# Kernel tuning notes

Hardware: AMD Instinct MI355X
Metric: run time of the kernel (lower is better)

The kernel has to match this reference:

```python
import jax, jax.numpy as jnp
import numpy as np

B, C, H, W = 2, 16, 160, 192
S, D = 3, 48
MIN_DEPTH, MAX_DEPTH = 0.5, 10.0
EPS = 1e-6


def setup_inputs() -> dict:
    key = jax.random.key(0)
    k1, k2 = jax.random.split(key)
    ref_feats = jax.random.normal(k1, (B, C, H, W), jnp.float32)
    src_feats = jax.random.normal(k2, (S, B, C, H, W), jnp.float32)
    K = np.array([[200.0, 0.0, W / 2.0], [0.0, 200.0, H / 2.0], [0.0, 0.0, 1.0]], np.float32)
    ref_intrinsics = jnp.broadcast_to(jnp.asarray(K), (B, 3, 3))
    src_intrinsics = jnp.broadcast_to(jnp.asarray(K), (S, B, 3, 3))
    T = np.tile(np.eye(4, dtype=np.float32), (S, B, 1, 1))
    T[:, :, 0, 3] = np.array([0.15, -0.15, 0.05], np.float32)[:, None]  # x baselines
    T[:, :, 1, 3] = 0.05  # small y offset
    ref_to_src = jnp.asarray(T)
    depth_hypotheses = jnp.linspace(MIN_DEPTH, MAX_DEPTH, D, dtype=jnp.float32)
    return {"ref_feats": ref_feats, "src_feats": src_feats,
            "ref_intrinsics": ref_intrinsics, "src_intrinsics": src_intrinsics,
            "ref_to_src": ref_to_src, "depth_hypotheses": depth_hypotheses}


def _bilinear(img, x, y, valid):
    """img: [B,C,Hs,Ws]; x,y,valid: [B,D,N]. Zero padding outside. -> [B,C,D,N]"""
    Hs, Ws = img.shape[2], img.shape[3]
    x0 = jnp.floor(x); y0 = jnp.floor(y)
    fx = x - x0; fy = y - y0
    x0i = x0.astype(jnp.int32); y0i = y0.astype(jnp.int32)
    gather = jax.vmap(lambda im, yy, xx: im[:, yy, xx])  # per-batch [C,D,N]
    out = jnp.zeros(img.shape[:2] + x.shape[1:], img.dtype)
    for dy in (0, 1):
        for dx in (0, 1):
            xi = x0i + dx; yi = y0i + dy
            w = (fx if dx else 1.0 - fx) * (fy if dy else 1.0 - fy)
            ok = valid & (xi >= 0) & (xi < Ws) & (yi >= 0) & (yi < Hs)
            vals = gather(img, jnp.clip(yi, 0, Hs - 1), jnp.clip(xi, 0, Ws - 1))
            out = out + vals * jnp.where(ok, w, 0.0)[:, None]
    return out


def _ncc(f1, f2, eps=EPS):
    """NCC over channel axis 1. f1: [B,C,1,H,W], f2: [B,C,D,H,W] -> [B,D,H,W]"""
    f1 = f1 - f1.mean(axis=1, keepdims=True)
    f2 = f2 - f2.mean(axis=1, keepdims=True)
    num = (f1 * f2).sum(axis=1)
    den = jnp.sqrt((f1 * f1).sum(axis=1)) * jnp.sqrt((f2 * f2).sum(axis=1)) + eps
    return num / den


def reference(ref_feats, src_feats, ref_intrinsics, src_intrinsics, ref_to_src, depth_hypotheses):
    b, c, h, w = ref_feats.shape
    s = src_feats.shape[0]
    us, vs = jnp.meshgrid(jnp.arange(w, dtype=jnp.float32), jnp.arange(h, dtype=jnp.float32))  # [h,w]
    pix = jnp.stack([us.ravel(), vs.ravel(), jnp.ones(h * w, jnp.float32)], axis=0)  # [3,HW]
    rays = jnp.einsum('bij,jn->bin', jnp.linalg.inv(ref_intrinsics), pix)  # [B,3,HW]
    X = depth_hypotheses[None, :, None, None] * rays[:, None]  # [B,D,3,HW]
    cost = jnp.zeros((b, depth_hypotheses.shape[0], h, w), ref_feats.dtype)
    for si in range(s):
        R = ref_to_src[si, :, :3, :3]; t = ref_to_src[si, :, :3, 3]
        Xs = jnp.einsum('bij,bdjn->bdin', R, X) + t[:, None, :, None]  # [B,D,3,HW]
        p = jnp.einsum('bij,bdjn->bdin', src_intrinsics[si], Xs)
        z = p[:, :, 2]
        valid = z > 1e-3
        zs = jnp.maximum(z, 1e-3)
        x = p[:, :, 0] / zs; y = p[:, :, 1] / zs  # [B,D,HW]
        warped = _bilinear(src_feats[si], x, y, valid).reshape(b, c, -1, h, w)  # [B,C,D,H,W]
        cost = cost + _ncc(ref_feats[:, :, None], warped)
    return cost / s
```

## Files before the change

kernel.cpp:

```cpp
#include <hip/hip_runtime.h>
#include <math.h>

constexpr int B = 2, C = 16, H = 160, W = 192, S = 3, D = 48;
constexpr int HW = H * W;

__global__ __launch_bounds__(256) void plane_sweep_kernel(
    const float* __restrict__ ref_feats,
    const float* __restrict__ src_feats,
    const float* __restrict__ ref_intr,
    const float* __restrict__ src_intr,
    const float* __restrict__ ref_to_src,
    const float* __restrict__ depths,
    float* __restrict__ out)
{
    const int idx = blockIdx.x * blockDim.x + threadIdx.x;
    const int total = B * D * HW;
    if (idx >= total) return;

    const int w = idx % W;
    const int h = (idx / W) % H;
    const int d = (idx / HW) % D;
    const int b = idx / (HW * D);

    const float* Kp = ref_intr + b * 9;
    const double a00 = Kp[0], a01 = Kp[1], a02 = Kp[2];
    const double a10 = Kp[3], a11 = Kp[4], a12 = Kp[5];
    const double a20 = Kp[6], a21 = Kp[7], a22 = Kp[8];
    const double cof00 =  (a11 * a22 - a12 * a21);
    const double cof01 = -(a10 * a22 - a12 * a20);
    const double cof02 =  (a10 * a21 - a11 * a20);
    const double cof10 = -(a01 * a22 - a02 * a21);
    const double cof11 =  (a00 * a22 - a02 * a20);
    const double cof12 = -(a00 * a21 - a01 * a20);
    const double cof20 =  (a01 * a12 - a02 * a11);
    const double cof21 = -(a00 * a12 - a02 * a10);
    const double cof22 =  (a00 * a11 - a01 * a10);
    const double det = a00 * cof00 + a01 * cof01 + a02 * cof02;
    const double invdet = 1.0 / det;
    const double i00 = cof00 * invdet, i01 = cof10 * invdet, i02 = cof20 * invdet;
    const double i10 = cof01 * invdet, i11 = cof11 * invdet, i12 = cof21 * invdet;
    const double i20 = cof02 * invdet, i21 = cof12 * invdet, i22 = cof22 * invdet;

    const double u = (double)w;
    const double v = (double)h;
    const double rayx = i00 * u + i01 * v + i02;
    const double rayy = i10 * u + i11 * v + i12;
    const double rayz = i20 * u + i21 * v + i22;

    const double depth = (double)depths[d];
    const double X0 = depth * rayx;
    const double X1 = depth * rayy;
    const double X2 = depth * rayz;

    float f1[C];
    const float* rp = ref_feats + (b * C) * HW + h * W + w;
    float sum1 = 0.0f;
    #pragma unroll
    for (int c = 0; c < C; ++c) {
        f1[c] = rp[c * HW];
        sum1 += f1[c];
    }
    const float m1 = sum1 * (1.0f / C);
    float sq1 = 0.0f;
    #pragma unroll
    for (int c = 0; c < C; ++c) {
        f1[c] -= m1;
        sq1 += f1[c] * f1[c];
    }
    const float n1 = sqrtf(sq1);

    float cost = 0.0f;

    for (int s = 0; s < S; ++s) {
        const float* Tp  = ref_to_src + (s * B + b) * 16;
        const float* Ksp = src_intr   + (s * B + b) * 9;

        const double Xsx = (double)Tp[0] * X0 + (double)Tp[1] * X1 + (double)Tp[2]  * X2 + (double)Tp[3];
        const double Xsy = (double)Tp[4] * X0 + (double)Tp[5] * X1 + (double)Tp[6]  * X2 + (double)Tp[7];
        const double Xsz = (double)Tp[8] * X0 + (double)Tp[9] * X1 + (double)Tp[10] * X2 + (double)Tp[11];

        const double p0 = (double)Ksp[0] * Xsx + (double)Ksp[1] * Xsy + (double)Ksp[2] * Xsz;
        const double p1 = (double)Ksp[3] * Xsx + (double)Ksp[4] * Xsy + (double)Ksp[5] * Xsz;
        const double p2 = (double)Ksp[6] * Xsx + (double)Ksp[7] * Xsy + (double)Ksp[8] * Xsz;

        const bool valid = p2 > 0.001;
        const double zs = fmax(p2, 0.001);
        const double invz = 1.0 / zs;
        const double x = p0 * invz;
        const double y = p1 * invz;

        const double x0f = floor(x);
        const double y0f = floor(y);
        const double fx = x - x0f;
        const double fy = y - y0f;
        const int x0 = (int)x0f;
        const int y0 = (int)y0f;
        const int x1 = x0 + 1;
        const int y1 = y0 + 1;

        double dw00 = (1.0 - fx) * (1.0 - fy);
        double dw01 = fx * (1.0 - fy);
        double dw10 = (1.0 - fx) * fy;
        double dw11 = fx * fy;
        const bool okx0 = (x0 >= 0) && (x0 < W);
        const bool okx1 = (x1 >= 0) && (x1 < W);
        const bool oky0 = (y0 >= 0) && (y0 < H);
        const bool oky1 = (y1 >= 0) && (y1 < H);
        const float w00 = (float)((valid && okx0 && oky0) ? dw00 : 0.0);
        const float w01 = (float)((valid && okx1 && oky0) ? dw01 : 0.0);
        const float w10 = (float)((valid && okx0 && oky1) ? dw10 : 0.0);
        const float w11 = (float)((valid && okx1 && oky1) ? dw11 : 0.0);

        const int x0c = min(max(x0, 0), W - 1);
        const int x1c = min(max(x1, 0), W - 1);
        const int y0c = min(max(y0, 0), H - 1);
        const int y1c = min(max(y1, 0), H - 1);

        const int off00 = y0c * W + x0c;
        const int off01 = y0c * W + x1c;
        const int off10 = y1c * W + x0c;
        const int off11 = y1c * W + x1c;

        const float* base = src_feats + ((size_t)(s * B + b) * C) * HW;

        float f2[C];
        float sum2 = 0.0f;
        #pragma unroll
        for (int c = 0; c < C; ++c) {
            const float* p = base + c * HW;
            const float v00 = p[off00];
            const float v01 = p[off01];
            const float v10 = p[off10];
            const float v11 = p[off11];
            const float val = w00 * v00 + w01 * v01 + w10 * v10 + w11 * v11;
            f2[c] = val;
            sum2 += val;
        }
        const float m2 = sum2 * (1.0f / C);
        float sq2 = 0.0f;
        float dot = 0.0f;
        #pragma unroll
        for (int c = 0; c < C; ++c) {
            const float f2c = f2[c] - m2;
            sq2 = fmaf(f2c, f2c, sq2);
            dot = fmaf(f1[c], f2c, dot);
        }
        const float den = n1 * sqrtf(sq2) + 1e-6f;
        cost += dot / den;
    }

    out[idx] = cost * (1.0f / S);
}

extern "C" void kernel_launch(void* const* d_in, const int* in_sizes, int n_in,
                              void* d_out, int out_size, void* d_ws, size_t ws_size,
                              hipStream_t stream) {
    const float* ref_feats  = (const float*)d_in[0];
    const float* src_feats  = (const float*)d_in[1];
    const float* ref_intr   = (const float*)d_in[2];
    const float* src_intr   = (const float*)d_in[3];
    const float* ref_to_src = (const float*)d_in[4];
    const float* depths     = (const float*)d_in[5];
    float* out = (float*)d_out;

    const int total = B * D * H * W;
    const int block = 256;
    const int grid = (total + block - 1) / block;
    plane_sweep_kernel<<<grid, block, 0, stream>>>(
        ref_feats, src_feats, ref_intr, src_intr, ref_to_src, depths, out);
}
```

Before: 185.4 us.

## Precompute combined projection matrices and process four depths per thread

Adds a tiny kernel that folds K_src·R·K_ref^-1 and K_src·t into per-(source,batch) 3x4 double matrices, so each pixel computes its projection as depth*ray + offset. Each thread now handles four depth hypotheses, reusing the reference-feature load, the normalization and the per-source ray setup across them. The double division is replaced by a hardware reciprocal with two Newton refinements. In exchange it cuts thread count fourfold, which may reduce memory-latency hiding for the gathers, and adds an extra kernel launch. Regrouping the arithmetic may also round slightly differently from the reference.

```diff
diff --git a/kernel.cpp b/kernel.cpp
--- a/kernel.cpp
+++ b/kernel.cpp
@@ -3,153 +3,183 @@
 
 constexpr int B = 2, C = 16, H = 160, W = 192, S = 3, D = 48;
 constexpr int HW = H * W;
-
-__global__ __launch_bounds__(256) void plane_sweep_kernel(
-    const float* __restrict__ ref_feats,
-    const float* __restrict__ src_feats,
-    const float* __restrict__ ref_intr,
-    const float* __restrict__ src_intr,
-    const float* __restrict__ ref_to_src,
-    const float* __restrict__ depths,
-    float* __restrict__ out)
+constexpr int ND = 4;
+constexpr int G = D / ND;
+
+__global__ void precompute_mats(const float* __restrict__ ref_intr,
+                                const float* __restrict__ src_intr,
+                                const float* __restrict__ ref_to_src,
+                                double* __restrict__ ws)
 {
-    const int idx = blockIdx.x * blockDim.x + threadIdx.x;
-    const int total = B * D * HW;
-    if (idx >= total) return;
-
-    const int w = idx % W;
-    const int h = (idx / W) % H;
-    const int d = (idx / HW) % D;
-    const int b = idx / (HW * D);
+    const int i = threadIdx.x;
+    if (i >= S * B) return;
+    const int b = i % B;
 
     const float* Kp = ref_intr + b * 9;
     const double a00 = Kp[0], a01 = Kp[1], a02 = Kp[2];
     const double a10 = Kp[3], a11 = Kp[4], a12 = Kp[5];
     const double a20 = Kp[6], a21 = Kp[7], a22 = Kp[8];
-    const double cof00 =  (a11 * a22 - a12 * a21);
-    const double cof01 = -(a10 * a22 - a12 * a20);
-    const double cof02 =  (a10 * a21 - a11 * a20);
-    const double cof10 = -(a01 * a22 - a02 * a21);
-    const double cof11 =  (a00 * a22 - a02 * a20);
-    const double cof12 = -(a00 * a21 - a01 * a20);
-    const double cof20 =  (a01 * a12 - a02 * a11);
-    const double cof21 = -(a00 * a12 - a02 * a10);
-    const double cof22 =  (a00 * a11 - a01 * a10);
-    const double det = a00 * cof00 + a01 * cof01 + a02 * cof02;
-    const double invdet = 1.0 / det;
-    const double i00 = cof00 * invdet, i01 = cof10 * invdet, i02 = cof20 * invdet;
-    const double i10 = cof01 * invdet, i11 = cof11 * invdet, i12 = cof21 * invdet;
-    const double i20 = cof02 * invdet, i21 = cof12 * invdet, i22 = cof22 * invdet;
-
-    const double u = (double)w;
-    const double v = (double)h;
-    const double rayx = i00 * u + i01 * v + i02;
-    const double rayy = i10 * u + i11 * v + i12;
-    const double rayz = i20 * u + i21 * v + i22;
-
-    const double depth = (double)depths[d];
-    const double X0 = depth * rayx;
-    const double X1 = depth * rayy;
-    const double X2 = depth * rayz;
+    const double c00 =  (a11 * a22 - a12 * a21);
+    const double c01 = -(a10 * a22 - a12 * a20);
+    const double c02 =  (a10 * a21 - a11 * a20);
+    const double c10 = -(a01 * a22 - a02 * a21);
+    const double c11 =  (a00 * a22 - a02 * a20);
+    const double c12 = -(a00 * a21 - a01 * a20);
+    const double c20 =  (a01 * a12 - a02 * a11);
+    const double c21 = -(a00 * a12 - a02 * a10);
+    const double c22 =  (a00 * a11 - a01 * a10);
+    const double invdet = 1.0 / (a00 * c00 + a01 * c01 + a02 * c02);
+    const double iK[9] = { c00 * invdet, c10 * invdet, c20 * invdet,
+                           c01 * invdet, c11 * invdet, c21 * invdet,
+                           c02 * invdet, c12 * invdet, c22 * invdet };
+
+    const float* Tp = ref_to_src + i * 16;
+    const float* Ks = src_intr + i * 9;
+
+    double M[9];
+    #pragma unroll
+    for (int r = 0; r < 3; ++r)
+        #pragma unroll
+        for (int c = 0; c < 3; ++c)
+            M[r * 3 + c] = (double)Tp[r * 4 + 0] * iK[0 + c]
+                         + (double)Tp[r * 4 + 1] * iK[3 + c]
+                         + (double)Tp[r * 4 + 2] * iK[6 + c];
+
+    double* o = ws + i * 12;
+    #pragma unroll
+    for (int r = 0; r < 3; ++r) {
+        #pragma unroll
+        for (int c = 0; c < 3; ++c)
+            o[r * 3 + c] = (double)Ks[r * 3 + 0] * M[0 + c]
+                         + (double)Ks[r * 3 + 1] * M[3 + c]
+                         + (double)Ks[r * 3 + 2] * M[6 + c];
+        o[9 + r] = (double)Ks[r * 3 + 0] * (double)Tp[3]
+                 + (double)Ks[r * 3 + 1] * (double)Tp[7]
+                 + (double)Ks[r * 3 + 2] * (double)Tp[11];
+    }
+}
+
+__global__ __launch_bounds__(256) void plane_sweep_kernel(
+    const float* __restrict__ ref_feats,
+    const float* __restrict__ src_feats,
+    const float* __restrict__ depths,
+    const double* __restrict__ ws,
+    float* __restrict__ out)
+{
+    const int idx = blockIdx.x * blockDim.x + threadIdx.x;
+    const int total = B * G * HW;
+    if (idx >= total) return;
+
+    const int w  = idx % W;
+    const int h  = (idx / W) % H;
+    const int dg = (idx / HW) % G;
+    const int b  = idx / (HW * G);
 
     float f1[C];
     const float* rp = ref_feats + (b * C) * HW + h * W + w;
     float sum1 = 0.0f;
     #pragma unroll
-    for (int c = 0; c < C; ++c) {
-        f1[c] = rp[c * HW];
-        sum1 += f1[c];
-    }
+    for (int c = 0; c < C; ++c) { f1[c] = rp[c * HW]; sum1 += f1[c]; }
     const float m1 = sum1 * (1.0f / C);
     float sq1 = 0.0f;
     #pragma unroll
-    for (int c = 0; c < C; ++c) {
-        f1[c] -= m1;
-        sq1 += f1[c] * f1[c];
+    for (int c = 0; c < C; ++c) { f1[c] -= m1; sq1 = fmaf(f1[c], f1[c], sq1); }
+    const float n1 = sqrtf(sq1);
+
+    const double u = (double)w, v = (double)h;
+    double rx[S], ry[S], rz[S], q0[S], q1[S], q2[S];
+    #pragma unroll
+    for (int s = 0; s < S; ++s) {
+        const double* Aq = ws + (s * B + b) * 12;
+        rx[s] = Aq[0] * u + Aq[1] * v + Aq[2];
+        ry[s] = Aq[3] * u + Aq[4] * v + Aq[5];
+        rz[s] = Aq[6] * u + Aq[7] * v + Aq[8];
+        q0[s] = Aq[9]; q1[s] = Aq[10]; q2[s] = Aq[11];
     }
-    const float n1 = sqrtf(sq1);
-
-    float cost = 0.0f;
-
-    for (int s = 0; s < S; ++s) {
-        const float* Tp  = ref_to_src + (s * B + b) * 16;
-        const float* Ksp = src_intr   + (s * B + b) * 9;
-
-        const double Xsx = (double)Tp[0] * X0 + (double)Tp[1] * X1 + (double)Tp[2]  * X2 + (double)Tp[3];
-        const double Xsy = (double)Tp[4] * X0 + (double)Tp[5] * X1 + (double)Tp[6]  * X2 + (double)Tp[7];
-        const double Xsz = (double)Tp[8] * X0 + (double)Tp[9] * X1 + (double)Tp[10] * X2 + (double)Tp[11];
-
-        const double p0 = (double)Ksp[0] * Xsx + (double)Ksp[1] * Xsy + (double)Ksp[2] * Xsz;
-        const double p1 = (double)Ksp[3] * Xsx + (double)Ksp[4] * Xsy + (double)Ksp[5] * Xsz;
-        const double p2 = (double)Ksp[6] * Xsx + (double)Ksp[7] * Xsy + (double)Ksp[8] * Xsz;
-
-        const bool valid = p2 > 0.001;
-        const double zs = fmax(p2, 0.001);
-        const double invz = 1.0 / zs;
-        const double x = p0 * invz;
-        const double y = p1 * invz;
-
-        const double x0f = floor(x);
-        const double y0f = floor(y);
-        const double fx = x - x0f;
-        const double fy = y - y0f;
-        const int x0 = (int)x0f;
-        const int y0 = (int)y0f;
-        const int x1 = x0 + 1;
-        const int y1 = y0 + 1;
-
-        double dw00 = (1.0 - fx) * (1.0 - fy);
-        double dw01 = fx * (1.0 - fy);
-        double dw10 = (1.0 - fx) * fy;
-        double dw11 = fx * fy;
-        const bool okx0 = (x0 >= 0) && (x0 < W);
-        const bool okx1 = (x1 >= 0) && (x1 < W);
-        const bool oky0 = (y0 >= 0) && (y0 < H);
-        const bool oky1 = (y1 >= 0) && (y1 < H);
-        const float w00 = (float)((valid && okx0 && oky0) ? dw00 : 0.0);
-        const float w01 = (float)((valid && okx1 && oky0) ? dw01 : 0.0);
-        const float w10 = (float)((valid && okx0 && oky1) ? dw10 : 0.0);
-        const float w11 = (float)((valid && okx1 && oky1) ? dw11 : 0.0);
-
-        const int x0c = min(max(x0, 0), W - 1);
-        const int x1c = min(max(x1, 0), W - 1);
-        const int y0c = min(max(y0, 0), H - 1);
-        const int y1c = min(max(y1, 0), H - 1);
-
-        const int off00 = y0c * W + x0c;
-        const int off01 = y0c * W + x1c;
-        const int off10 = y1c * W + x0c;
-        const int off11 = y1c * W + x1c;
-
-        const float* base = src_feats + ((size_t)(s * B + b) * C) * HW;
-
-        float f2[C];
-        float sum2 = 0.0f;
+
+    float* op = out + (size_t)((b * D + dg * ND) * HW + h * W + w);
+
+    #pragma unroll 1
+    for (int j = 0; j < ND; ++j) {
+        const double depth = (double)depths[dg * ND + j];
+        float cost = 0.0f;
+
         #pragma unroll
-        for (int c = 0; c < C; ++c) {
-            const float* p = base + c * HW;
-            const float v00 = p[off00];
-            const float v01 = p[off01];
-            const float v10 = p[off10];
-            const float v11 = p[off11];
-            const float val = w00 * v00 + w01 * v01 + w10 * v10 + w11 * v11;
-            f2[c] = val;
-            sum2 += val;
+        for (int s = 0; s < S; ++s) {
+            const double p0 = fma(depth, rx[s], q0[s]);
+            const double p1 = fma(depth, ry[s], q1[s]);
+            const double p2 = fma(depth, rz[s], q2[s]);
+
+            const bool valid = p2 > 0.001;
+            const double zs = fmax(p2, 0.001);
+#if __has_builtin(__builtin_amdgcn_rcp)
+            double r = __builtin_amdgcn_rcp(zs);
+#else
+            double r = (double)__builtin_amdgcn_rcpf((float)zs);
+#endif
+            r = r * fma(-zs, r, 2.0);
+            r = r * fma(-zs, r, 2.0);
+            const double x = p0 * r;
+            const double y = p1 * r;
+
+            const double x0f = floor(x);
+            const double y0f = floor(y);
+            const double fx = x - x0f;
+            const double fy = y - y0f;
+            const int x0 = (int)x0f;
+            const int y0 = (int)y0f;
+            const int x1 = x0 + 1;
+            const int y1 = y0 + 1;
+
+            const double gx = 1.0 - fx, gy = 1.0 - fy;
+            const bool okx0 = (x0 >= 0) & (x0 < W);
+            const bool okx1 = (x1 >= 0) & (x1 < W);
+            const bool oky0 = (y0 >= 0) & (y0 < H);
+            const bool oky1 = (y1 >= 0) & (y1 < H);
+            const float w00 = (float)((valid & okx0 & oky0) ? gx * gy : 0.0);
+            const float w01 = (float)((valid & okx1 & oky0) ? fx * gy : 0.0);
+            const float w10 = (float)((valid & okx0 & oky1) ? gx * fy : 0.0);
+            const float w11 = (float)((valid & okx1 & oky1) ? fx * fy : 0.0);
+
+            const int x0c = min(max(x0, 0), W - 1);
+            const int x1c = min(max(x1, 0), W - 1);
+            const int y0c = min(max(y0, 0), H - 1);
+            const int y1c = min(max(y1, 0), H - 1);
+            const int off00 = y0c * W + x0c;
+            const int off01 = y0c * W + x1c;
+            const int off10 = y1c * W + x0c;
+            const int off11 = y1c * W + x1c;
+
+            const float* base = src_feats + ((size_t)(s * B + b) * C) * HW;
+
+            float f2[C];
+            float sum2 = 0.0f;
+            #pragma unroll
+            for (int c = 0; c < C; ++c) {
+                const float* p = base + c * HW;
+                const float v00 = p[off00];
+                const float v01 = p[off01];
+                const float v10 = p[off10];
+                const float v11 = p[off11];
+                const float val = w00 * v00 + w01 * v01 + w10 * v10 + w11 * v11;
+                f2[c] = val;
+                sum2 += val;
+            }
+            const float m2 = sum2 * (1.0f / C);
+            float sq2 = 0.0f;
+            float dot = 0.0f;
+            #pragma unroll
+            for (int c = 0; c < C; ++c) {
+                const float f2c = f2[c] - m2;
+                sq2 = fmaf(f2c, f2c, sq2);
+                dot = fmaf(f1[c], f2c, dot);
+            }
+            const float den = n1 * sqrtf(sq2) + 1e-6f;
+            cost += dot / den;
         }
-        const float m2 = sum2 * (1.0f / C);
-        float sq2 = 0.0f;
-        float dot = 0.0f;
-        #pragma unroll
-        for (int c = 0; c < C; ++c) {
-            const float f2c = f2[c] - m2;
-            sq2 = fmaf(f2c, f2c, sq2);
-            dot = fmaf(f1[c], f2c, dot);
-        }
-        const float den = n1 * sqrtf(sq2) + 1e-6f;
-        cost += dot / den;
+
+        op[j * HW] = cost * (1.0f / S);
     }
-
-    out[idx] = cost * (1.0f / S);
 }
 
 extern "C" void kernel_launch(void* const* d_in, const int* in_sizes, int n_in,
@@ -162,10 +192,13 @@
     const float* ref_to_src = (const float*)d_in[4];
     const float* depths     = (const float*)d_in[5];
     float* out = (float*)d_out;
-
-    const int total = B * D * H * W;
+    double* ws = (double*)d_ws;
+
+    precompute_mats<<<1, 64, 0, stream>>>(ref_intr, src_intr, ref_to_src, ws);
+
+    const int total = B * G * HW;
     const int block = 256;
     const int grid = (total + block - 1) / block;
     plane_sweep_kernel<<<grid, block, 0, stream>>>(
-        ref_feats, src_feats, ref_intr, src_intr, ref_to_src, depths, out);
+        ref_feats, src_feats, depths, ws, out);
 }
```

New measurement: 335.3 us. 80.8% more time.
